# Kernel optimization log

Measured on AMD Instinct MI355X. Metric: run time of the kernel, lower is better.

The kernel has to match this reference:

```python
import math
import jax, jax.numpy as jnp
import numpy as np

D = 1024        # d_model
N = 32          # order // 2 modes
SEQ = 4096      # kernel length L
DT_MIN, DT_MAX = 1e-3, 1e-1


def setup_inputs() -> dict:
    key = jax.random.key(0)
    k1, k2 = jax.random.split(key)
    # log_dt ~ Uniform[log(dt_min), log(dt_max)]
    log_dt = jax.random.uniform(k1, (D,), jnp.float32) * (math.log(DT_MAX) - math.log(DT_MIN)) + math.log(DT_MIN)
    # C stored as view_as_real: (1, D, N, 2)
    C_ri = jax.random.normal(k2, (1, D, N, 2), jnp.float32)
    # inv_A_real = log(-A.real) = log(0.5)
    inv_A_real = jnp.full((D, N), math.log(0.5), dtype=jnp.float32)
    # A_imag = pi * arange(N) broadcast over d_model
    A_imag = math.pi * jnp.broadcast_to(jnp.arange(N, dtype=jnp.float32), (D, N))
    return {"log_dt": log_dt, "C_ri": C_ri, "inv_A_real": inv_A_real, "A_imag": A_imag, "L": SEQ}


def reference(log_dt, C_ri, inv_A_real, A_imag, L):
    dt = jnp.exp(log_dt)                                   # (D,)
    C = jax.lax.complex(C_ri[..., 0], C_ri[..., 1])        # (1, D, N) complex64
    A = jax.lax.complex(-jnp.exp(inv_A_real), A_imag)      # (D, N) complex64
    dtA = A * dt[:, None]                                  # (D, N)
    # Vandermonde: exp(dtA * l) for l in [0, L) -> (D, N, L) complex, the big intermediate
    K = jnp.exp(dtA[:, :, None] * jnp.arange(L, dtype=jnp.float32))
    # reduce over modes n: h = 2 * Re( sum_n C[z,d,n] * K[d,n,l] )
    h = 2.0 * jnp.real(jnp.einsum('zdn,dnl->zdl', C, K))   # (1, D, L)
    return h
```

## Files before the change

kernel.cpp:

```cpp
#include <hip/hip_runtime.h>
#include <hip/hip_bf16.h>
#include <math.h>


constexpr int D_MODEL = 1024;
constexpr int NMODES  = 32;
constexpr int SEQLEN  = 4096;

typedef _Float16 half8 __attribute__((ext_vector_type(8)));
typedef float    f32x4 __attribute__((ext_vector_type(4)));

__global__ __launch_bounds__(256, 1)
void modal_mfma_kernel(const float* __restrict__ log_dt,
                       const float* __restrict__ C_ri,
                       const float* __restrict__ inv_A_real,
                       const float* __restrict__ A_imag,
                       float* __restrict__ out)
{
    const int wave = threadIdx.x >> 6;
    const int lane = threadIdx.x & 63;
    const int d    = blockIdx.x * 4 + wave;
    const int g    = lane >> 4;
    const int q    = lane & 15;
    const float qf = (float)q;

    const float dt = __expf(log_dt[d]);

    half8 Sr[4], Si[4], Tr[4], Tin[4];

#pragma unroll
    for (int e = 0; e < 8; ++e) {
        const int k   = 8 * g + e;
        const int idx = d * NMODES + k;
        const float a   = -__expf(inv_A_real[idx]) * dt;
        const float b   = A_imag[idx] * dt;
        const float cr2 = 2.0f * C_ri[2 * idx + 0];
        const float ci2 = 2.0f * C_ri[2 * idx + 1];

        float s, c;
        float ea = __expf(a * qf);
        __sincosf(b * qf, &s, &c);
        float pr = ea * (cr2 * c - ci2 * s);
        float pi = ea * (cr2 * s + ci2 * c);
        float s16, c16;
        float e16 = __expf(16.0f * a);
        __sincosf(16.0f * b, &s16, &c16);
        float xr = e16 * c16, xi = e16 * s16;
        float sq, cq;
        float eq = __expf(64.0f * a * qf);
        __sincosf(64.0f * b * qf, &sq, &cq);
        float tr = eq * cq, ti = eq * sq;
        float s1k, c1k;
        float e1k = __expf(1024.0f * a);
        __sincosf(1024.0f * b, &s1k, &c1k);
        float yr = e1k * c1k, yi = e1k * s1k;

#pragma unroll
        for (int t = 0; t < 4; ++t) {
            Sr[t][e]  = (_Float16)pr;
            Si[t][e]  = (_Float16)pi;
            Tr[t][e]  = (_Float16)tr;
            Tin[t][e] = (_Float16)(-ti);
            float npr = pr * xr - pi * xi;  pi = pr * xi + pi * xr;  pr = npr;
            float ntr = tr * yr - ti * yi;  ti = tr * yi + ti * yr;  tr = ntr;
        }
    }

    float* od = out + (size_t)d * SEQLEN;
#pragma unroll
    for (int ti = 0; ti < 4; ++ti) {
#pragma unroll
        for (int tj = 0; tj < 4; ++tj) {
            f32x4 acc = {0.f, 0.f, 0.f, 0.f};
            acc = __builtin_amdgcn_mfma_f32_16x16x32_f16(Sr[ti], Tr[tj],  acc, 0, 0, 0);
            acc = __builtin_amdgcn_mfma_f32_16x16x32_f16(Si[ti], Tin[tj], acc, 0, 0, 0);
            const int i = ti * 16 + 4 * g;
            const int j = tj * 16 + q;
            *reinterpret_cast<f32x4*>(od + (size_t)j * 64 + i) = acc;
        }
    }
}

extern "C" void kernel_launch(void* const* d_in, const int* in_sizes, int n_in,
                              void* d_out, int out_size, void* d_ws, size_t ws_size,
                              hipStream_t stream) {
    const float* log_dt     = (const float*)d_in[0];
    const float* C_ri       = (const float*)d_in[1];
    const float* inv_A_real = (const float*)d_in[2];
    const float* A_imag     = (const float*)d_in[3];
    float* out              = (float*)d_out;

    modal_mfma_kernel<<<D_MODEL / 4, 256, 0, stream>>>(log_dt, C_ri, inv_A_real, A_imag, out);
}
```

Measured before the change: 11.32 us.

## Split each channel across two waves and use a 16x256 time factorization

Changes the L=4096 factorization from 64x64 (four S tiles by four T tiles) to 16x256 (one S tile, sixteen T tiles). Each channel is now split across two waves that each compute eight output tiles, which doubles the grid. The T powers are advanced with a complex recurrence in fp32 before converting to fp16 per tile, and launch bounds allow two blocks per CU. The goal is more parallelism and fewer live registers, at the cost of duplicating the per-mode setup transcendentals across waves and using a longer recurrence chain, which may affect accuracy.

Result: faster. 10.96 us (-3.2%).

```diff
diff --git a/kernel.cpp b/kernel.cpp
--- a/kernel.cpp
+++ b/kernel.cpp
@@ -6,27 +6,32 @@
 constexpr int D_MODEL = 1024;
 constexpr int NMODES  = 32;
 constexpr int SEQLEN  = 4096;
+constexpr int WAVES_PER_D = 2;
+constexpr int TILES_PER_WAVE = 16 / WAVES_PER_D;
 
 typedef _Float16 half8 __attribute__((ext_vector_type(8)));
 typedef float    f32x4 __attribute__((ext_vector_type(4)));
 
-__global__ __launch_bounds__(256, 1)
+__global__ __launch_bounds__(256, 2)
 void modal_mfma_kernel(const float* __restrict__ log_dt,
                        const float* __restrict__ C_ri,
                        const float* __restrict__ inv_A_real,
                        const float* __restrict__ A_imag,
                        float* __restrict__ out)
 {
-    const int wave = threadIdx.x >> 6;
+    const int wave = (blockIdx.x * 256 + (int)threadIdx.x) >> 6;
     const int lane = threadIdx.x & 63;
-    const int d    = blockIdx.x * 4 + wave;
+    const int d    = wave / WAVES_PER_D;
+    const int half = wave % WAVES_PER_D;
+    const int tj0  = half * TILES_PER_WAVE;
     const int g    = lane >> 4;
     const int q    = lane & 15;
     const float qf = (float)q;
 
     const float dt = __expf(log_dt[d]);
 
-    half8 Sr[4], Si[4], Tr[4], Tin[4];
+    half8 Sr, Si;
+    float wr[8], wi[8], yr[8], yi[8];
 
 #pragma unroll
     for (int e = 0; e < 8; ++e) {
@@ -38,46 +43,42 @@
         const float ci2 = 2.0f * C_ri[2 * idx + 1];
 
         float s, c;
-        float ea = __expf(a * qf);
+        const float ea = __expf(a * qf);
         __sincosf(b * qf, &s, &c);
-        float pr = ea * (cr2 * c - ci2 * s);
-        float pi = ea * (cr2 * s + ci2 * c);
-        float s16, c16;
-        float e16 = __expf(16.0f * a);
-        __sincosf(16.0f * b, &s16, &c16);
-        float xr = e16 * c16, xi = e16 * s16;
-        float sq, cq;
-        float eq = __expf(64.0f * a * qf);
-        __sincosf(64.0f * b * qf, &sq, &cq);
-        float tr = eq * cq, ti = eq * sq;
-        float s1k, c1k;
-        float e1k = __expf(1024.0f * a);
-        __sincosf(1024.0f * b, &s1k, &c1k);
-        float yr = e1k * c1k, yi = e1k * s1k;
+        Sr[e] = (_Float16)(ea * (cr2 * c - ci2 * s));
+        Si[e] = (_Float16)(ea * (cr2 * s + ci2 * c));
+
+        const float j0 = 16.0f * (16.0f * (float)tj0 + qf);
+        float sw, cw;
+        const float ew = __expf(a * j0);
+        __sincosf(b * j0, &sw, &cw);
+        wr[e] = ew * cw;
+        wi[e] = ew * sw;
+
+        float sy, cy;
+        const float ey = __expf(256.0f * a);
+        __sincosf(256.0f * b, &sy, &cy);
+        yr[e] = ey * cy;
+        yi[e] = ey * sy;
+    }
+
+    float* od = out + (size_t)d * SEQLEN + 256 * tj0 + 16 * q + 4 * g;
 
 #pragma unroll
-        for (int t = 0; t < 4; ++t) {
-            Sr[t][e]  = (_Float16)pr;
-            Si[t][e]  = (_Float16)pi;
-            Tr[t][e]  = (_Float16)tr;
-            Tin[t][e] = (_Float16)(-ti);
-            float npr = pr * xr - pi * xi;  pi = pr * xi + pi * xr;  pr = npr;
-            float ntr = tr * yr - ti * yi;  ti = tr * yi + ti * yr;  tr = ntr;
+    for (int t = 0; t < TILES_PER_WAVE; ++t) {
+        half8 Trh, Tih;
+#pragma unroll
+        for (int e = 0; e < 8; ++e) {
+            Trh[e] = (_Float16)wr[e];
+            Tih[e] = (_Float16)(-wi[e]);
+            const float nr = wr[e] * yr[e] - wi[e] * yi[e];
+            wi[e] = wr[e] * yi[e] + wi[e] * yr[e];
+            wr[e] = nr;
         }
-    }
-
-    float* od = out + (size_t)d * SEQLEN;
-#pragma unroll
-    for (int ti = 0; ti < 4; ++ti) {
-#pragma unroll
-        for (int tj = 0; tj < 4; ++tj) {
-            f32x4 acc = {0.f, 0.f, 0.f, 0.f};
-            acc = __builtin_amdgcn_mfma_f32_16x16x32_f16(Sr[ti], Tr[tj],  acc, 0, 0, 0);
-            acc = __builtin_amdgcn_mfma_f32_16x16x32_f16(Si[ti], Tin[tj], acc, 0, 0, 0);
-            const int i = ti * 16 + 4 * g;
-            const int j = tj * 16 + q;
-            *reinterpret_cast<f32x4*>(od + (size_t)j * 64 + i) = acc;
-        }
+        f32x4 acc = {0.f, 0.f, 0.f, 0.f};
+        acc = __builtin_amdgcn_mfma_f32_16x16x32_f16(Sr, Trh, acc, 0, 0, 0);
+        acc = __builtin_amdgcn_mfma_f32_16x16x32_f16(Si, Tih, acc, 0, 0, 0);
+        *reinterpret_cast<f32x4*>(od + 256 * t) = acc;
     }
 }
 
@@ -90,5 +91,6 @@
     const float* A_imag     = (const float*)d_in[3];
     float* out              = (float*)d_out;
 
-    modal_mfma_kernel<<<D_MODEL / 4, 256, 0, stream>>>(log_dt, C_ri, inv_A_real, A_imag, out);
+    modal_mfma_kernel<<<D_MODEL * WAVES_PER_D / 4, 256, 0, stream>>>(
+        log_dt, C_ri, inv_A_real, A_imag, out);
 }
```
